# Optimization experiments

Measured on AMD Instinct MI355X. Metric: run time of the kernel, lower is better.

## Reference

```python
import jax, jax.numpy as jnp
import numpy as np

# Mamba2 hyperparameters
D_MODEL = 768
D_STATE = 64
D_CONV = 4
EXPAND = 2
HEADDIM = 64
CHUNK = 64
D_INNER = EXPAND * D_MODEL            # 1536
NHEADS = D_INNER // HEADDIM           # 24
D_IN_PROJ = 2 * D_INNER + 2 * D_STATE + NHEADS  # 3224
CONV_DIM = D_INNER + 2 * D_STATE      # 1664
B_SZ = 8
SEQ = 4096  # multiple of CHUNK -> no padding branch


def setup_inputs() -> dict:
    key = jax.random.key(0)
    ks = jax.random.split(key, 6)
    u = jax.random.normal(ks[0], (B_SZ, SEQ, D_MODEL), jnp.float32)
    # fan-in scaled weights (matches nn.Linear/Conv1d default init scale)
    W_in = jax.random.normal(ks[1], (D_IN_PROJ, D_MODEL), jnp.float32) / np.sqrt(D_MODEL).astype(np.float32)
    conv_w = jax.random.normal(ks[2], (CONV_DIM, 1, D_CONV), jnp.float32) / np.sqrt(D_CONV).astype(np.float32)
    conv_b = jnp.zeros((CONV_DIM,), jnp.float32)
    dt_bias = jax.random.uniform(ks[3], (NHEADS,), jnp.float32, -4.0, 1.0)  # nn.init.uniform_(-4, 1)
    A_log = jnp.full((NHEADS,), -np.log(2.0), jnp.float32)                  # nn.init.constant_(-log 2)
    D_param = jnp.ones((NHEADS,), jnp.float32)
    norm_w = jnp.ones((D_INNER,), jnp.float32)
    W_out = jax.random.normal(ks[4], (D_MODEL, D_INNER), jnp.float32) / np.sqrt(D_INNER).astype(np.float32)
    return dict(u=u, W_in=W_in, conv_w=conv_w, conv_b=conv_b, dt_bias=dt_bias,
                A_log=A_log, D_param=D_param, norm_w=norm_w, W_out=W_out)


def _segsum(x):
    """Stable segment sum: out[..., i, j] = sum_{j < k <= i} x[..., k]; -inf above diagonal."""
    T = x.shape[-1]
    lower_strict = jnp.tril(jnp.ones((T, T), bool), -1)
    xe = jnp.where(lower_strict, x[..., :, None], 0.0)   # broadcast x over last (col) axis
    s = jnp.cumsum(xe, axis=-2)
    lower = jnp.tril(jnp.ones((T, T), bool), 0)
    return jnp.where(lower, s, -jnp.inf)


def _ssd(x, A, B, C, chunk):
    """Chunked SSD. x:(b,L,h,p)  A:(b,L,h)  B,C:(b,L,1,n)."""
    b, L, h, p = x.shape
    c = L // chunk
    n = B.shape[-1]
    x = x.reshape(b, c, chunk, h, p)
    A = A.reshape(b, c, chunk, h).transpose(0, 3, 1, 2)   # b h c l
    B = B.reshape(b, c, chunk, 1, n)
    C = C.reshape(b, c, chunk, 1, n)
    A_cs = jnp.cumsum(A, axis=-1)                          # b h c l
    # intra-chunk (diagonal) term
    Lmat = jnp.exp(_segsum(A))                             # b h c l s
    Y_diag = jnp.einsum('bclhn,bcshn,bhcls,bcshp->bclhp', C, B, Lmat, x)
    # per-chunk states
    decay_states = jnp.exp(A_cs[..., -1:] - A_cs)          # b h c l
    states = jnp.einsum('bclhn,bhcl,bclhp->bchpn', B, decay_states, x)
    states = jnp.concatenate([jnp.zeros_like(states[:, :1]), states], axis=1)  # b (c+1) h p n
    # inter-chunk recurrence
    A_last = jnp.pad(A_cs[..., -1], ((0, 0), (0, 0), (1, 0)))  # b h (c+1)
    decay_chunk = jnp.exp(_segsum(A_last))                     # b h (c+1) (c+1)
    new_states = jnp.einsum('bhzc,bchpn->bzhpn', decay_chunk, states)
    states = new_states[:, :-1]                                # b c h p n
    # off-diagonal (state-to-output) term
    Y_off = jnp.einsum('bclhn,bchpn,bhcl->bclhp', C, states, jnp.exp(A_cs))
    return (Y_diag + Y_off).reshape(b, L, h, p)


def reference(u, W_in, conv_w, conv_b, dt_bias, A_log, D_param, norm_w, W_out):
    b, L, _ = u.shape  # L % CHUNK == 0, so pad branch is a no-op
    zxbcdt = u @ W_in.T                                    # (b, L, D_IN_PROJ)
    z = zxbcdt[..., :D_INNER]
    xBC = zxbcdt[..., D_INNER:D_INNER + CONV_DIM]
    dt = jax.nn.softplus(zxbcdt[..., D_INNER + CONV_DIM:] + dt_bias)  # (b, L, h)
    # causal depthwise conv1d (torch pads both sides by d_conv-1 then slices [:L] == left pad)
    xBC = jax.lax.conv_general_dilated(
        xBC.transpose(0, 2, 1), conv_w, window_strides=(1,),
        padding=[(D_CONV - 1, 0)], dimension_numbers=('NCH', 'OIH', 'NCH'),
        feature_group_count=CONV_DIM)
    xBC = jax.nn.silu(xBC.transpose(0, 2, 1) + conv_b)     # (b, L, CONV_DIM)
    x = xBC[..., :D_INNER].reshape(b, L, NHEADS, HEADDIM)
    Bm = xBC[..., D_INNER:D_INNER + D_STATE][:, :, None, :]  # (b, L, 1, n)
    Cm = xBC[..., D_INNER + D_STATE:][:, :, None, :]
    A = -jnp.exp(A_log)                                    # (h,)
    Y = _ssd(x * dt[..., None], A * dt, Bm, Cm, CHUNK)
    y = Y + x * D_param[:, None]                           # skip term
    y = y.reshape(b, L, D_INNER)
    # gated RMSNorm: x * silu(z), then rmsnorm * weight
    y = y * jax.nn.silu(z)
    y = y * jax.lax.rsqrt(jnp.mean(y * y, axis=-1, keepdims=True) + 1e-5) * norm_w
    return y @ W_out.T
```

## Files before the change

kernel.cpp:

```cpp
#include <hip/hip_runtime.h>
#include <stdint.h>

typedef unsigned short u16;
typedef __bf16 bf16x8 __attribute__((ext_vector_type(8)));
typedef float f32x4 __attribute__((ext_vector_type(4)));
typedef unsigned short u16x8 __attribute__((ext_vector_type(8)));
typedef unsigned short u16x4 __attribute__((ext_vector_type(4)));
typedef __attribute__((address_space(1))) unsigned int gu32;
typedef __attribute__((address_space(3))) unsigned int lu32;

__device__ __forceinline__ float bf2f(u16 u){ unsigned int v=((unsigned int)u)<<16; float f; __builtin_memcpy(&f,&v,4); return f; }
__device__ __forceinline__ u16 f2bf(float f){ unsigned int v; __builtin_memcpy(&v,&f,4); v += 0x7fffu + ((v>>16)&1u); return (u16)(v>>16); }
__device__ __forceinline__ int swz(int r,int c){ return (r<<6) + (c ^ ((r&7)<<3)); }
__device__ __forceinline__ void glds16(const void* g, void* l){
  __builtin_amdgcn_global_load_lds((gu32*)g, (lu32*)l, 16, 0, 0);
}

__global__ __launch_bounds__(256) void k_cast(const float* __restrict__ in, u16* __restrict__ out, int n4){
  int i = blockIdx.x*256 + threadIdx.x;
  if (i >= n4) return;
  const f32x4 v = *(const f32x4*)(in + (size_t)i*4);
  u16x4 o; o.x=f2bf(v.x); o.y=f2bf(v.y); o.z=f2bf(v.z); o.w=f2bf(v.w);
  *(u16x4*)(out + (size_t)i*4) = o;
}

__global__ __launch_bounds__(256) void k_cast_pad(const float* __restrict__ in, u16* __restrict__ out){
  int i = blockIdx.x*256 + threadIdx.x;
  int e0 = i*4;
  int row = e0 / 768;
  int col = e0 - row*768;
  u16x4 o;
  if (row < 3224){
    const f32x4 v = *(const f32x4*)(in + (size_t)row*768 + col);
    o.x=f2bf(v.x); o.y=f2bf(v.y); o.z=f2bf(v.z); o.w=f2bf(v.w);
  } else { o.x=0; o.y=0; o.z=0; o.w=0; }
  *(u16x4*)(out + e0) = o;
}

template<int K, int EPI>
__global__ __launch_bounds__(256,2) void k_gemm(
    const u16* __restrict__ A, const u16* __restrict__ Bw,
    u16* __restrict__ o_z, u16* __restrict__ o_xbc, float* __restrict__ o_dt,
    const float* __restrict__ dt_bias, float* __restrict__ o_f32)
{
  __shared__ __align__(16) u16 Alds[8192];
  __shared__ __align__(16) u16 Blds[8192];
  const int tid = threadIdx.x;
  const int wave = tid>>6, lane = tid&63;
  const int m0 = blockIdx.x<<7, n0 = blockIdx.y<<7;
  const int wr = (wave>>1)<<6, wc = (wave&1)<<6;
  const int srow = tid>>3, sc0 = (tid&7)<<3;
  const int lo16 = lane&15, hi = lane>>4;
  f32x4 acc[4][4] = {};
  for (int k0 = 0; k0 < K; k0 += 64){
    #pragma unroll
    for (int i = 0; i < 4; ++i){
      const int row = (i<<5) + srow;
      const int scol = sc0 ^ ((row&7)<<3);
      glds16(A  + (size_t)(m0+row)*K + k0 + scol, &Alds[(i<<11) + (wave<<9)]);
      glds16(Bw + (size_t)(n0+row)*K + k0 + scol, &Blds[(i<<11) + (wave<<9)]);
    }
    __syncthreads();
    #pragma unroll
    for (int kk = 0; kk < 2; ++kk){
      const int kb = (kk<<5) + (hi<<3);
      bf16x8 af[4], bfv[4];
      #pragma unroll
      for (int m = 0; m < 4; ++m){
        const int r = wr + (m<<4) + lo16;
        af[m] = *(const bf16x8*)&Alds[(r<<6) + (kb ^ ((r&7)<<3))];
      }
      #pragma unroll
      for (int n = 0; n < 4; ++n){
        const int r = wc + (n<<4) + lo16;
        bfv[n] = *(const bf16x8*)&Blds[(r<<6) + (kb ^ ((r&7)<<3))];
      }
      #pragma unroll
      for (int m = 0; m < 4; ++m)
      #pragma unroll
      for (int n = 0; n < 4; ++n)
        acc[m][n] = __builtin_amdgcn_mfma_f32_16x16x32_bf16(af[m], bfv[n], acc[m][n], 0,0,0);
    }
    __syncthreads();
  }
  #pragma unroll
  for (int m = 0; m < 4; ++m)
  #pragma unroll
  for (int n = 0; n < 4; ++n)
  #pragma unroll
  for (int i = 0; i < 4; ++i){
    const int gr = m0 + wr + (m<<4) + (hi<<2) + i;
    const int gc = n0 + wc + (n<<4) + lo16;
    const float v = acc[m][n][i];
    if constexpr (EPI == 0){
      if (gc < 1536)      o_z[(size_t)gr*1536 + gc] = f2bf(v);
      else if (gc < 3200) o_xbc[(size_t)gr*1664 + (gc-1536)] = f2bf(v);
      else if (gc < 3224){
        const float t = v + dt_bias[gc-3200];
        o_dt[(size_t)(gc-3200)*32768 + gr] = (t > 20.f) ? t : log1pf(__expf(t));
      }
    } else {
      o_f32[(size_t)gr*768 + gc] = v;
    }
  }
}

__global__ __launch_bounds__(256) void k_conv(
    const u16* __restrict__ xbc, const float* __restrict__ cw, const float* __restrict__ cb,
    const float* __restrict__ dtT,
    u16* __restrict__ xT, u16* __restrict__ Bn, u16* __restrict__ BT, u16* __restrict__ Cn)
{
  const int idx = blockIdx.x*256 + threadIdx.x;
  if (idx >= 4096*208) return;
  const int g  = idx % 208;
  const int pt = idx / 208;
  const int ch0 = g << 3;
  const int m0 = pt << 3;
  const int l0 = m0 & 4095;
  float wgt[8][4], bias8[8];
  #pragma unroll
  for (int j = 0; j < 8; ++j){
    const f32x4 wv = *(const f32x4*)(cw + (size_t)(ch0+j)*4);
    wgt[j][0]=wv.x; wgt[j][1]=wv.y; wgt[j][2]=wv.z; wgt[j][3]=wv.w;
    bias8[j] = cb[ch0+j];
  }
  float acc[8][8];
  #pragma unroll
  for (int p = 0; p < 8; ++p)
  #pragma unroll
  for (int j = 0; j < 8; ++j) acc[p][j] = bias8[j];
  #pragma unroll
  for (int r = -3; r < 8; ++r){
    const int ls = l0 + r;
    if (ls < 0) continue;
    const u16x8 v = *(const u16x8*)(xbc + (size_t)(m0+r)*1664 + ch0);
    float xf[8];
    #pragma unroll
    for (int j = 0; j < 8; ++j) xf[j] = bf2f(v[j]);
    #pragma unroll
    for (int t = 0; t < 4; ++t){
      const int p = r + 3 - t;
      if (p < 0 || p > 7) continue;
      #pragma unroll
      for (int j = 0; j < 8; ++j) acc[p][j] += xf[j] * wgt[j][t];
    }
  }
  #pragma unroll
  for (int p = 0; p < 8; ++p)
  #pragma unroll
  for (int j = 0; j < 8; ++j){ const float s = acc[p][j]; acc[p][j] = s / (1.f + __expf(-s)); }

  const int b = m0 >> 12;
  const int cch = l0 >> 6;
  const int lr0 = l0 & 63;
  if (ch0 < 1536){
    const int h = ch0 >> 6, p0 = ch0 & 63;
    const f32x4 d0 = *(const f32x4*)(dtT + (size_t)h*32768 + m0);
    const f32x4 d1 = *(const f32x4*)(dtT + (size_t)h*32768 + m0 + 4);
    const float dtl[8] = {d0.x,d0.y,d0.z,d0.w,d1.x,d1.y,d1.z,d1.w};
    const size_t rb = (size_t)(b*24+h)*64;
    #pragma unroll
    for (int j = 0; j < 8; ++j){
      const int row = p0 + j;
      u16x8 o;
      #pragma unroll
      for (int p = 0; p < 8; ++p) o[p] = f2bf(acc[p][j] * dtl[p]);
      *(u16x8*)(xT + (rb + row)*4096 + (size_t)cch*64 + (lr0 ^ ((row&7)<<3))) = o;
    }
  } else if (ch0 < 1600){
    const int n0 = ch0 - 1536;
    const size_t tb = ((size_t)(b*64 + cch))*4096;
    #pragma unroll
    for (int p = 0; p < 8; ++p){
      const int lr = lr0 + p;
      u16x8 o;
      #pragma unroll
      for (int j = 0; j < 8; ++j) o[j] = f2bf(acc[p][j]);
      *(u16x8*)(Bn + tb + lr*64 + (n0 ^ ((lr&7)<<3))) = o;
    }
    #pragma unroll
    for (int j = 0; j < 8; ++j){
      const int row = n0 + j;
      u16x8 o;
      #pragma unroll
      for (int p = 0; p < 8; ++p) o[p] = f2bf(acc[p][j]);
      *(u16x8*)(BT + tb + row*64 + (lr0 ^ ((row&7)<<3))) = o;
    }
  } else {
    const int n0 = ch0 - 1600;
    const size_t tb = ((size_t)(b*64 + cch))*4096;
    #pragma unroll
    for (int p = 0; p < 8; ++p){
      const int lr = lr0 + p;
      u16x8 o;
      #pragma unroll
      for (int j = 0; j < 8; ++j) o[j] = f2bf(acc[p][j]);
      *(u16x8*)(Cn + tb + lr*64 + (n0 ^ ((lr&7)<<3))) = o;
    }
  }
}

__global__ __launch_bounds__(256,1) void k_ssd(
    const u16* __restrict__ xT, const u16* __restrict__ Bn, const u16* __restrict__ BT,
    const u16* __restrict__ Cn, const float* __restrict__ dtT, const float* __restrict__ A_log,
    const float* __restrict__ Dp, u16* __restrict__ yo)
{
  __shared__ __align__(16) u16 tiles[2][4][4096];
  __shared__ __align__(16) u16 Ml[4096];
  __shared__ __align__(16) u16 Sbf[4096];
  const int tid = threadIdx.x, wave = tid>>6, lane = tid&63;
  const int lo16 = lane&15, hi = lane>>4;
  const int w16 = wave<<4, hi4 = hi<<2;
  const int b = blockIdx.x / 24, h = blockIdx.x % 24;
  const float Ah = -__expf(A_log[h]);
  const float Dh = Dp[h];
  for (int i = tid; i < 4096; i += 256) Sbf[i] = 0;
  f32x4 Sreg[4] = {};
  const size_t xTg  = (size_t)(b*24+h)*64*4096;
  const size_t bcg  = (size_t)b*64*4096;
  const size_t dtg0 = (size_t)h*32768 + (size_t)b*4096;
  const size_t yb   = (size_t)b*4096*1536 + (size_t)h*64;

  auto stage = [&](int buf, int c){
    u16* dst = &tiles[buf][wave][0];
    if (wave == 0){
      const u16* g0 = xT + xTg + (size_t)c*64 + (size_t)(lane>>3)*4096 + (lane&7)*8;
      #pragma unroll
      for (int s = 0; s < 8; ++s) glds16(g0 + (size_t)s*32768, dst + s*512);
    } else {
      const u16* src = (wave==1 ? Bn : wave==2 ? BT : Cn) + bcg + (size_t)c*4096 + lane*8;
      #pragma unroll
      for (int s = 0; s < 8; ++s) glds16(src + s*512, dst + s*512);
    }
  };

  float dtc = dtT[dtg0 + lane];
  stage(0, 0);

  for (int c = 0; c < 64; ++c){
    float s = Ah * dtc;
    #pragma unroll
    for (int o = 1; o < 64; o <<= 1){ const float t = __shfl_up(s, o); if (lane >= o) s += t; }
    const float Alast = __shfl(s, 63);
    const float lam  = __expf(Alast);
    const float decl = __expf(Alast - s);
    const float elv  = __expf(s);
    float dtn = 0.f;
    if (c < 63){
      dtn = dtT[dtg0 + (size_t)(c+1)*64 + lane];
      stage((c+1)&1, c+1);
    }
    if (c == 0)       asm volatile("s_waitcnt vmcnt(9)  lgkmcnt(0)" ::: "memory");
    else if (c == 63) asm volatile("s_waitcnt vmcnt(4)  lgkmcnt(0)" ::: "memory");
    else              asm volatile("s_waitcnt vmcnt(13) lgkmcnt(0)" ::: "memory");
    __builtin_amdgcn_s_barrier();

    const u16* tx = &tiles[c&1][0][0];
    const u16* tb = &tiles[c&1][1][0];
    const u16* tt = &tiles[c&1][2][0];
    const u16* tc = &tiles[c&1][3][0];

    f32x4 accG[4] = {};
    bf16x8 bfC[2][4];
    #pragma unroll
    for (int kk = 0; kk < 2; ++kk){
      const int kb = (kk<<5) + (hi<<3);
      const int rA = w16 + lo16;
      const bf16x8 aB = *(const bf16x8*)&tb[(rA<<6) + (kb ^ ((rA&7)<<3))];
      #pragma unroll
      for (int t = 0; t < 4; ++t){
        const int rb = (t<<4) + lo16;
        bfC[kk][t] = *(const bf16x8*)&tc[(rb<<6) + (kb ^ ((rb&7)<<3))];
        accG[t] = __builtin_amdgcn_mfma_f32_16x16x32_bf16(aB, bfC[kk][t], accG[t], 0,0,0);
      }
    }
    float As_i[4];
    #pragma unroll
    for (int i = 0; i < 4; ++i) As_i[i] = __shfl(s, w16 + hi4 + i);
    #pragma unroll
    for (int t = 0; t < 4; ++t){
      const int l = (t<<4) + lo16;
      const float Al  = __shfl(s, l);
      const float dtl = __shfl(dtc, l);
      u16x4 ov;
      #pragma unroll
      for (int i = 0; i < 4; ++i){
        const int si = w16 + hi4 + i;
        float v = 0.f;
        if (si <= l) v = accG[t][i] * __expf(Al - As_i[i]);
        if (si == l) v += Dh / dtl;
        ov[i] = f2bf(v);
      }
      *(u16x4*)&Ml[(l<<6) + ((w16 + hi4) ^ ((l&7)<<3))] = ov;
    }
    asm volatile("s_waitcnt lgkmcnt(0)" ::: "memory");
    __builtin_amdgcn_s_barrier();

    f32x4 aYd[4] = {}, aYo[4] = {}, aS[4] = {};
    #pragma unroll
    for (int kk = 0; kk < 2; ++kk){
      const int kb = (kk<<5) + (hi<<3);
      const int rA = w16 + lo16;
      const int oA = (rA<<6) + (kb ^ ((rA&7)<<3));
      const bf16x8 aX = *(const bf16x8*)&tx[oA];
      const bf16x8 aSb= *(const bf16x8*)&Sbf[oA];
      const u16x8 aBTu= *(const u16x8*)&tt[oA];
      u16x8 aBTs;
      #pragma unroll
      for (int j = 0; j < 8; ++j) aBTs[j] = f2bf(bf2f(aBTu[j]) * __shfl(decl, kb + j));
      const bf16x8 aBT = *(const bf16x8*)&aBTs;
      #pragma unroll
      for (int t = 0; t < 4; ++t){
        const int rb = (t<<4) + lo16;
        const int o = (rb<<6) + (kb ^ ((rb&7)<<3));
        const bf16x8 bM = *(const bf16x8*)&Ml[o];
        const bf16x8 bX = *(const bf16x8*)&tx[o];
        aYd[t] = __builtin_amdgcn_mfma_f32_16x16x32_bf16(aX,  bM,         aYd[t], 0,0,0);
        aYo[t] = __builtin_amdgcn_mfma_f32_16x16x32_bf16(aSb, bfC[kk][t], aYo[t], 0,0,0);
        aS[t]  = __builtin_amdgcn_mfma_f32_16x16x32_bf16(aBT, bX,         aS[t],  0,0,0);
      }
    }
    asm volatile("s_waitcnt lgkmcnt(0)" ::: "memory");
    __builtin_amdgcn_s_barrier();

    #pragma unroll
    for (int t = 0; t < 4; ++t){
      const int p = (t<<4) + lo16;
      u16x4 sv;
      #pragma unroll
      for (int i = 0; i < 4; ++i){
        const float nv = Sreg[t][i] * lam + aS[t][i];
        Sreg[t][i] = nv;
        sv[i] = f2bf(nv);
      }
      *(u16x4*)&Sbf[(p<<6) + ((w16 + hi4) ^ ((p&7)<<3))] = sv;
    }
    #pragma unroll
    for (int t = 0; t < 4; ++t){
      const int l = (t<<4) + lo16;
      const float el = elv;
      (void)el;
      const float elt = __shfl(elv, l);
      u16x4 ov;
      #pragma unroll
      for (int i = 0; i < 4; ++i) ov[i] = f2bf(aYd[t][i] + elt * aYo[t][i]);
      *(u16x4*)(yo + yb + (size_t)((c<<6)+l)*1536 + w16 + hi4) = ov;
    }
    dtc = dtn;
  }
}

__global__ __launch_bounds__(192) void k_gnorm(
    const u16* __restrict__ y, const u16* __restrict__ z,
    const float* __restrict__ nw, u16* __restrict__ out)
{
  __shared__ float red[3];
  const int m = blockIdx.x, t = threadIdx.x;
  const size_t base = (size_t)m*1536 + t*8;
  const u16x8 yv = *(const u16x8*)(y + base);
  const u16x8 zv = *(const u16x8*)(z + base);
  float vals[8]; float ss = 0.f;
  #pragma unroll
  for (int j = 0; j < 8; ++j){
    const float zf = bf2f(zv[j]);
    const float v = bf2f(yv[j]) * zf / (1.f + __expf(-zf));
    vals[j] = v; ss += v*v;
  }
  #pragma unroll
  for (int off = 32; off > 0; off >>= 1) ss += __shfl_down(ss, off);
  if ((t & 63) == 0) red[t>>6] = ss;
  __syncthreads();
  const float sc = rsqrtf((red[0]+red[1]+red[2]) * (1.f/1536.f) + 1e-5f);
  u16x8 o;
  #pragma unroll
  for (int j = 0; j < 8; ++j) o[j] = f2bf(vals[j] * sc * nw[t*8+j]);
  *(u16x8*)(out + base) = o;
}

extern "C" void kernel_launch(void* const* d_in, const int* in_sizes, int n_in,
                              void* d_out, int out_size, void* d_ws, size_t ws_size,
                              hipStream_t stream)
{
  const float* u       = (const float*)d_in[0];
  const float* W_in    = (const float*)d_in[1];
  const float* conv_w  = (const float*)d_in[2];
  const float* conv_b  = (const float*)d_in[3];
  const float* dt_bias = (const float*)d_in[4];
  const float* A_log   = (const float*)d_in[5];
  const float* D_param = (const float*)d_in[6];
  const float* norm_w  = (const float*)d_in[7];
  const float* W_out   = (const float*)d_in[8];
  (void)in_sizes; (void)n_in; (void)out_size;
  if (ws_size < (size_t)379715584) return;

  char* w = (char*)d_ws;
  size_t off = 0;
  auto alloc = [&](size_t bytes)->void*{ void* p = w + off; off += (bytes + 255) & ~(size_t)255; return p; };
  u16* ubf    = (u16*)alloc(50331648);
  u16* winbf  = (u16*)alloc(5111808);
  u16* woutbf = (u16*)alloc(2359296);
  u16* zbf    = (u16*)alloc(100663296);
  u16* xbcbf  = (u16*)alloc(109051904);
  float* dtT  = (float*)alloc(3145728);
  u16* xTb    = (u16*)alloc(100663296);
  u16* Bnb    = (u16*)alloc(4194304);
  u16* Cnb    = (u16*)alloc(4194304);
  u16* BTb    = ubf;
  u16* yssd   = xbcbf;
  u16* ynorm  = xTb;

  k_cast<<<24576, 256, 0, stream>>>(u, ubf, 6291456);
  k_cast_pad<<<2496, 256, 0, stream>>>(W_in, winbf);
  k_cast<<<1152, 256, 0, stream>>>(W_out, woutbf, 294912);
  k_gemm<768,0><<<dim3(256,26), 256, 0, stream>>>(ubf, winbf, zbf, xbcbf, dtT, dt_bias, nullptr);
  k_conv<<<3328, 256, 0, stream>>>(xbcbf, conv_w, conv_b, dtT, xTb, Bnb, BTb, Cnb);
  k_ssd<<<192, 256, 0, stream>>>(xTb, Bnb, BTb, Cnb, dtT, A_log, D_param, yssd);
  k_gnorm<<<32768, 192, 0, stream>>>(yssd, zbf, norm_w, ynorm);
  k_gemm<1536,1><<<dim3(256,6), 256, 0, stream>>>(ynorm, woutbf, nullptr, nullptr, nullptr, nullptr, (float*)d_out);
}
```

Before: 738.1 us.

## Pipeline GEMM with triple-buffered LDS, 256x128 tiles and XCD block remap

Restructures both projection GEMMs to use 512-thread blocks computing 256x128 tiles with a three-stage asynchronous global-to-LDS prefetch pipeline, replacing the single-buffered load/sync loop. Block IDs are remapped so that neighbouring tiles land on the same XCD to improve L2 reuse, and MFMA sections are raised in wave priority. This is meant to hide global load latency behind matrix math. In exchange it uses much more LDS, which limits occupancy to about one block per CU.

Result: slower. 807.5 us (+9.4%).

```diff
diff --git a/kernel.cpp b/kernel.cpp
--- a/kernel.cpp
+++ b/kernel.cpp
@@ -37,51 +37,75 @@
   *(u16x4*)(out + e0) = o;
 }
 
-template<int K, int EPI>
-__global__ __launch_bounds__(256,2) void k_gemm(
+template<int K, int NT, int EPI>
+__global__ __launch_bounds__(512,2) void k_gemm(
     const u16* __restrict__ A, const u16* __restrict__ Bw,
     u16* __restrict__ o_z, u16* __restrict__ o_xbc, float* __restrict__ o_dt,
     const float* __restrict__ dt_bias, float* __restrict__ o_f32)
 {
-  __shared__ __align__(16) u16 Alds[8192];
-  __shared__ __align__(16) u16 Blds[8192];
+  __shared__ __align__(16) u16 As[3][16384];
+  __shared__ __align__(16) u16 Bs[3][8192];
   const int tid = threadIdx.x;
   const int wave = tid>>6, lane = tid&63;
-  const int m0 = blockIdx.x<<7, n0 = blockIdx.y<<7;
-  const int wr = (wave>>1)<<6, wc = (wave&1)<<6;
-  const int srow = tid>>3, sc0 = (tid&7)<<3;
   const int lo16 = lane&15, hi = lane>>4;
+  const int nwg = 128*NT;
+  const int cpx = nwg>>3;
+  const int bid = (int)blockIdx.x;
+  const int sb  = (bid%8)*cpx + bid/8;
+  const int m0 = (sb/NT)<<8, n0 = (sb%NT)<<7;
+  const int wm = wave>>1, wn = wave&1;
+  constexpr int ntk = K/64;
+
+  auto stage = [&](int t){
+    const int buf = t%3; const int k0 = t<<6;
+    #pragma unroll
+    for (int s = 0; s < 4; ++s){
+      const int row = (wave<<5) + (s<<3) + (lane>>3);
+      const int scol = ((lane&7)<<3) ^ ((row&7)<<3);
+      glds16(A + (size_t)(m0+row)*K + k0 + scol, &As[buf][(((wave<<5)+(s<<3))<<6) + (lane<<3)]);
+    }
+    #pragma unroll
+    for (int s = 0; s < 2; ++s){
+      const int row = (wave<<4) + (s<<3) + (lane>>3);
+      const int scol = ((lane&7)<<3) ^ ((row&7)<<3);
+      glds16(Bw + (size_t)(n0+row)*K + k0 + scol, &Bs[buf][(((wave<<4)+(s<<3))<<6) + (lane<<3)]);
+    }
+  };
+
   f32x4 acc[4][4] = {};
-  for (int k0 = 0; k0 < K; k0 += 64){
-    #pragma unroll
-    for (int i = 0; i < 4; ++i){
-      const int row = (i<<5) + srow;
-      const int scol = sc0 ^ ((row&7)<<3);
-      glds16(A  + (size_t)(m0+row)*K + k0 + scol, &Alds[(i<<11) + (wave<<9)]);
-      glds16(Bw + (size_t)(n0+row)*K + k0 + scol, &Blds[(i<<11) + (wave<<9)]);
-    }
-    __syncthreads();
+  stage(0); stage(1);
+  for (int t = 0; t < ntk; ++t){
+    if (t == ntk-1) asm volatile("s_waitcnt vmcnt(0)" ::: "memory");
+    else            asm volatile("s_waitcnt vmcnt(6)" ::: "memory");
+    __builtin_amdgcn_s_barrier();
+    asm volatile("" ::: "memory");
+    if (t+2 < ntk) stage(t+2);
+    const u16* a = &As[t%3][0];
+    const u16* b = &Bs[t%3][0];
+    bf16x8 af[2][4], bfv[2][4];
     #pragma unroll
     for (int kk = 0; kk < 2; ++kk){
       const int kb = (kk<<5) + (hi<<3);
-      bf16x8 af[4], bfv[4];
       #pragma unroll
       for (int m = 0; m < 4; ++m){
-        const int r = wr + (m<<4) + lo16;
-        af[m] = *(const bf16x8*)&Alds[(r<<6) + (kb ^ ((r&7)<<3))];
+        const int r = (wm<<6) + (m<<4) + lo16;
+        af[kk][m] = *(const bf16x8*)&a[(r<<6) + (kb ^ ((r&7)<<3))];
       }
       #pragma unroll
       for (int n = 0; n < 4; ++n){
-        const int r = wc + (n<<4) + lo16;
-        bfv[n] = *(const bf16x8*)&Blds[(r<<6) + (kb ^ ((r&7)<<3))];
-      }
-      #pragma unroll
-      for (int m = 0; m < 4; ++m)
-      #pragma unroll
-      for (int n = 0; n < 4; ++n)
-        acc[m][n] = __builtin_amdgcn_mfma_f32_16x16x32_bf16(af[m], bfv[n], acc[m][n], 0,0,0);
-    }
-    __syncthreads();
+        const int r = (wn<<6) + (n<<4) + lo16;
+        bfv[kk][n] = *(const bf16x8*)&b[(r<<6) + (kb ^ ((r&7)<<3))];
+      }
+    }
+    __builtin_amdgcn_s_setprio(1);
+    #pragma unroll
+    for (int kk = 0; kk < 2; ++kk)
+    #pragma unroll
+    for (int m = 0; m < 4; ++m)
+    #pragma unroll
+    for (int n = 0; n < 4; ++n)
+      acc[m][n] = __builtin_amdgcn_mfma_f32_16x16x32_bf16(af[kk][m], bfv[kk][n], acc[m][n], 0,0,0);
+    __builtin_amdgcn_s_setprio(0);
   }
   #pragma unroll
   for (int m = 0; m < 4; ++m)
@@ -89,8 +113,8 @@
   for (int n = 0; n < 4; ++n)
   #pragma unroll
   for (int i = 0; i < 4; ++i){
-    const int gr = m0 + wr + (m<<4) + (hi<<2) + i;
-    const int gc = n0 + wc + (n<<4) + lo16;
+    const int gr = m0 + (wm<<6) + (m<<4) + (hi<<2) + i;
+    const int gc = n0 + (wn<<6) + (n<<4) + lo16;
     const float v = acc[m][n][i];
     if constexpr (EPI == 0){
       if (gc < 1536)      o_z[(size_t)gr*1536 + gc] = f2bf(v);
@@ -338,8 +362,6 @@
     #pragma unroll
     for (int t = 0; t < 4; ++t){
       const int l = (t<<4) + lo16;
-      const float el = elv;
-      (void)el;
       const float elt = __shfl(elv, l);
       u16x4 ov;
       #pragma unroll
@@ -412,9 +434,9 @@
   k_cast<<<24576, 256, 0, stream>>>(u, ubf, 6291456);
   k_cast_pad<<<2496, 256, 0, stream>>>(W_in, winbf);
   k_cast<<<1152, 256, 0, stream>>>(W_out, woutbf, 294912);
-  k_gemm<768,0><<<dim3(256,26), 256, 0, stream>>>(ubf, winbf, zbf, xbcbf, dtT, dt_bias, nullptr);
+  k_gemm<768,26,0><<<3328, 512, 0, stream>>>(ubf, winbf, zbf, xbcbf, dtT, dt_bias, nullptr);
   k_conv<<<3328, 256, 0, stream>>>(xbcbf, conv_w, conv_b, dtT, xTb, Bnb, BTb, Cnb);
   k_ssd<<<192, 256, 0, stream>>>(xTb, Bnb, BTb, Cnb, dtT, A_log, D_param, yssd);
   k_gnorm<<<32768, 192, 0, stream>>>(yssd, zbf, norm_w, ynorm);
-  k_gemm<1536,1><<<dim3(256,6), 256, 0, stream>>>(ynorm, woutbf, nullptr, nullptr, nullptr, nullptr, (float*)d_out);
-}
+  k_gemm<1536,6,1><<<768, 512, 0, stream>>>(ynorm, woutbf, nullptr, nullptr, nullptr, nullptr, (float*)d_out);
+}
```
